# Kernel optimization log

Hardware: AMD Instinct MI355X
Metric: run time of the kernel (lower is better)

Reference implementation:

```python
import jax, jax.numpy as jnp
import numpy as np

B, T, C = 4, 2048, 768
H, D = 12, 64          # num_heads, head_size
R = 64                 # kv_lora_rank
ROPE_THETA = 10000.0


def setup_inputs() -> dict:
    key = jax.random.key(0)
    ks = jax.random.split(key, 8)
    s = lambda fan_in: 1.0 / np.sqrt(fan_in)
    return {
        "x":      jax.random.normal(ks[0], (B, T, C), jnp.float32),
        "Wq":     jax.random.normal(ks[1], (C, H * D), jnp.float32) * s(C),
        "Wdown":  jax.random.normal(ks[2], (C, R), jnp.float32) * s(C),
        "ln_g":   jnp.ones((R,), jnp.float32),
        "ln_b":   jnp.zeros((R,), jnp.float32),
        "Wup":    jax.random.normal(ks[3], (R, 2 * H * D), jnp.float32) * s(R),
        "Wo":     jax.random.normal(ks[4], (H * D, C), jnp.float32) * s(H * D),
        "bo":     jnp.zeros((C,), jnp.float32),
    }


def _rope_cos_sin(t, d, dtype):
    # freqs over half-dim, repeated twice (rotate-half convention)
    inv_freq = 1.0 / (ROPE_THETA ** (jnp.arange(0, d, 2, dtype=jnp.float32) / d))
    ang = jnp.arange(t, dtype=jnp.float32)[:, None] * inv_freq[None, :]  # [T, D/2]
    ang = jnp.concatenate([ang, ang], axis=-1)                            # [T, D]
    return jnp.cos(ang).astype(dtype), jnp.sin(ang).astype(dtype)


def _apply_rope(q, cos, sin):
    # q: [B, H, T, D]; cos/sin: [T, D]
    d2 = q.shape[-1] // 2
    rot = jnp.concatenate([-q[..., d2:], q[..., :d2]], axis=-1)
    return q * cos + rot * sin


def reference(x, Wq, Wdown, ln_g, ln_b, Wup, Wo, bo):
    b, t, c = x.shape
    q = (x @ Wq).reshape(b, t, H, D).transpose(0, 2, 1, 3)  # [B,H,T,D]

    ckv = x @ Wdown                                         # [B,T,R]
    mu = jnp.mean(ckv, axis=-1, keepdims=True)
    var = jnp.var(ckv, axis=-1, keepdims=True)
    ckv = (ckv - mu) * jax.lax.rsqrt(var + 1e-5) * ln_g + ln_b

    kv = (ckv @ Wup).reshape(b, t, 2, H, D)
    k = kv[:, :, 0].transpose(0, 2, 1, 3)                   # [B,H,T,D]
    v = kv[:, :, 1].transpose(0, 2, 1, 3)

    cos, sin = _rope_cos_sin(t, D, x.dtype)
    q = _apply_rope(q, cos, sin)
    k = _apply_rope(k, cos, sin)

    wei = jnp.einsum("bhqd,bhkd->bhqk", q, k) * (D ** -0.5)
    causal = jnp.tril(jnp.ones((t, t), bool))
    wei = jnp.where(causal, wei, -jnp.inf)
    wei = jax.nn.softmax(wei, axis=-1)                      # dropout: eval mode (identity)

    out = jnp.einsum("bhqk,bhkd->bhqd", wei, v)             # [B,H,T,D]
    out = out.transpose(0, 2, 1, 3).reshape(b, t, H * D)
    return out @ Wo + bo
```

## Files before the change

kernel.cpp:

```cpp
#include <hip/hip_runtime.h>
#include <hip/hip_bf16.h>
#include <math.h>

#define B_ 4
#define T_ 2048
#define C_ 768
#define H_ 12
#define D_ 64
#define R_ 64
#define BT_ (B_*T_)
#define HD_ (H_*D_)

typedef __attribute__((ext_vector_type(8))) short bf16x8;
typedef __attribute__((ext_vector_type(4))) float f32x4;
typedef __attribute__((ext_vector_type(16))) float f32x16;

__device__ inline short f2bf(float f) {
  union { float f; unsigned u; } x; x.f = f;
  unsigned r = x.u + 0x7fffu + ((x.u >> 16) & 1u);
  return (short)(r >> 16);
}
__device__ inline unsigned pk_bf16(float a, float b) {
#if __has_builtin(__builtin_amdgcn_cvt_pk_bf16_f32)
  auto t = __builtin_amdgcn_cvt_pk_bf16_f32(a, b);
  unsigned u; __builtin_memcpy(&u, &t, sizeof(unsigned)); return u;
#else
  union { float f; unsigned u; } x, y; x.f = a; y.f = b;
  unsigned ra = (x.u + 0x7fffu + ((x.u >> 16) & 1u)) >> 16;
  unsigned rb = (y.u + 0x7fffu + ((y.u >> 16) & 1u)) & 0xffff0000u;
  return ra | rb;
#endif
}
__device__ inline float fexp2(float x) {
#if __has_builtin(__builtin_amdgcn_exp2f)
  return __builtin_amdgcn_exp2f(x);
#else
  return exp2f(x);
#endif
}
typedef __attribute__((address_space(3))) unsigned lds_u32;
typedef __attribute__((address_space(1))) const unsigned glb_u32;
__device__ inline void gload_lds16(const void* g, void* l) {
  __builtin_amdgcn_global_load_lds((glb_u32*)g, (lds_u32*)l, 16, 0, 0);
}

__device__ inline void ttile(const float* __restrict__ src, short* __restrict__ dst,
                             int K, int N, int k0, int n0, int tid, float (*tl)[33]) {
  int tx = tid & 31, ty = tid >> 5;
  #pragma unroll
  for (int r = 0; r < 4; ++r)
    tl[ty + 8 * r][tx] = src[(size_t)(k0 + ty + 8 * r) * N + n0 + tx];
  __syncthreads();
  #pragma unroll
  for (int r = 0; r < 4; ++r)
    dst[(size_t)(n0 + ty + 8 * r) * K + k0 + tx] = f2bf(tl[tx][ty + 8 * r]);
}

#define NCONV (BT_*C_/4/256)

__global__ __launch_bounds__(256) void prep_conv(
    const float* __restrict__ x, short* __restrict__ x_bf,
    const float* __restrict__ Wq, const float* __restrict__ Wd,
    const float* __restrict__ Wup, const float* __restrict__ Wo,
    short* __restrict__ W1T, short* __restrict__ WupT, short* __restrict__ WoT,
    float* __restrict__ cs, float* __restrict__ sn) {
  __shared__ float tl[32][33];
  int tid = threadIdx.x;
  if (blockIdx.x < NCONV) {
    int i = blockIdx.x * 256 + tid;
    float4 v = ((const float4*)x)[i];
    short4 o;
    o.x = f2bf(v.x); o.y = f2bf(v.y); o.z = f2bf(v.z); o.w = f2bf(v.w);
    ((short4*)x_bf)[i] = o;
    return;
  }
  int blk = blockIdx.x - NCONV;
  if (blk < 576) {
    int tk = blk % 24, tn = blk / 24;
    ttile(Wq, W1T, 768, 768, tk * 32, tn * 32, tid, tl);
  } else if (blk < 624) {
    int l = blk - 576; int tk = l % 24, tn = l / 24;
    ttile(Wd, W1T + (size_t)768 * 768, 768, 64, tk * 32, tn * 32, tid, tl);
  } else if (blk < 720) {
    int l = blk - 624; int tk = l % 2, tn = l / 2;
    ttile(Wup, WupT, 64, 1536, tk * 32, tn * 32, tid, tl);
  } else if (blk < 1296) {
    int l = blk - 720; int tk = l % 24, tn = l / 24;
    ttile(Wo, WoT, 768, 768, tk * 32, tn * 32, tid, tl);
  } else {
    int base = (blk - 1296) * 1024;
    #pragma unroll
    for (int i = 0; i < 4; ++i) {
      int idx = base + tid + i * 256;
      int j = idx & 31, t = idx >> 5;
      float invf = exp2f(-(float)j * (13.287712379549449f / 32.f));
      float a = (float)t * invf;
      cs[idx] = cosf(a);
      sn[idx] = sinf(a);
    }
  }
}

#define SC2_ 0.18033688f

template<int MODE>
__global__ __launch_bounds__(256) void gemm64(
    const short* __restrict__ A, const short* __restrict__ Bt,
    int M, int N, int K,
    float* __restrict__ out0, const float* __restrict__ bias,
    const float* __restrict__ bias2,
    short* __restrict__ ob0, short* __restrict__ ob1,
    const float* __restrict__ cs, const float* __restrict__ sn)
{
  __shared__ short SM[128 * 64 + 64 * 64];
  short* As = SM;
  short* Bs = SM + 128 * 64;
  const int m0 = blockIdx.x * 128;
  const int n0 = blockIdx.y * 64;
  const int tid = threadIdx.x, lane = tid & 63, w = tid >> 6;
  const int fr = lane & 15, fk = (lane >> 4) * 8;
  const int rstage = lane >> 3;
  const int cstage = (lane & 7) * 8;

  f32x4 acc[2][4] = {};

  for (int k0 = 0; k0 < K; k0 += 64) {
    __syncthreads();
    #pragma unroll
    for (int i = 0; i < 4; ++i) {
      int c = w * 4 + i;
      int r = c * 8 + rstage;
      gload_lds16(&A[(size_t)(m0 + r) * K + k0 + cstage], &As[c * 512]);
    }
    #pragma unroll
    for (int i = 0; i < 2; ++i) {
      int c = w * 2 + i;
      int r = c * 8 + rstage;
      gload_lds16(&Bt[(size_t)(n0 + r) * K + k0 + cstage], &Bs[c * 512]);
    }
    __syncthreads();
    #pragma unroll
    for (int kk = 0; kk < 64; kk += 32) {
      bf16x8 a[2], b[4];
      a[0] = *(const bf16x8*)&As[(w * 32 +      fr) * 64 + kk + fk];
      a[1] = *(const bf16x8*)&As[(w * 32 + 16 + fr) * 64 + kk + fk];
      #pragma unroll
      for (int ni = 0; ni < 4; ++ni)
        b[ni] = *(const bf16x8*)&Bs[(ni * 16 + fr) * 64 + kk + fk];
      #pragma unroll
      for (int mi = 0; mi < 2; ++mi)
        #pragma unroll
        for (int ni = 0; ni < 4; ++ni)
          acc[mi][ni] = __builtin_amdgcn_mfma_f32_16x16x32_bf16(a[mi], b[ni], acc[mi][ni], 0, 0, 0);
    }
  }

  const int er = (lane >> 4) * 4, ec = lane & 15;

  if constexpr (MODE == 2) {
    #pragma unroll
    for (int mi = 0; mi < 2; ++mi)
      #pragma unroll
      for (int r = 0; r < 4; ++r) {
        int row = m0 + w * 32 + mi * 16 + er + r;
        #pragma unroll
        for (int ni = 0; ni < 4; ++ni) {
          int col = n0 + ni * 16 + ec;
          out0[(size_t)row * N + col] = acc[mi][ni][r] + bias[col];
        }
      }
    return;
  }

  if (n0 < 768) {
    int h = n0 >> 6;
    #pragma unroll
    for (int mi = 0; mi < 2; ++mi)
      #pragma unroll
      for (int r = 0; r < 4; ++r) {
        int row = m0 + w * 32 + mi * 16 + er + r;
        int t = row & (T_ - 1), bb = row >> 11;
        short* dst = ob0 + (((size_t)(bb * H_ + h)) * T_ + t) * 64;
        #pragma unroll
        for (int ni = 0; ni < 2; ++ni) {
          int d = ni * 16 + ec;
          float c = cs[t * 32 + d], s = sn[t * 32 + d];
          if constexpr (MODE == 0) { c *= SC2_; s *= SC2_; }
          float x0 = acc[mi][ni][r], x1 = acc[mi][ni + 2][r];
          dst[d]      = f2bf(x0 * c - x1 * s);
          dst[d + 32] = f2bf(x1 * c + x0 * s);
        }
      }
  } else if constexpr (MODE == 0) {
    #pragma unroll
    for (int mi = 0; mi < 2; ++mi)
      #pragma unroll
      for (int r = 0; r < 4; ++r) {
        float s = 0.f, s2 = 0.f;
        #pragma unroll
        for (int ni = 0; ni < 4; ++ni) { float v = acc[mi][ni][r]; s += v; s2 += v*v; }
        #pragma unroll
        for (int off = 1; off < 16; off <<= 1) {
          s  += __shfl_xor(s, off);
          s2 += __shfl_xor(s2, off);
        }
        float mu = s * (1.f/64.f);
        float var = s2 * (1.f/64.f) - mu * mu;
        float rstd = rsqrtf(var + 1e-5f);
        int row = m0 + w * 32 + mi * 16 + er + r;
        #pragma unroll
        for (int ni = 0; ni < 4; ++ni) {
          int d = ni * 16 + ec;
          ob1[(size_t)row * 64 + d] = f2bf((acc[mi][ni][r] - mu) * rstd * bias[d] + bias2[d]);
        }
      }
  } else {
    __syncthreads();
    short* Wl = SM + w * 2560;
    int h = (n0 - 768) >> 6;
    #pragma unroll
    for (int mi = 0; mi < 2; ++mi) {
      int tl0 = mi * 16 + er;
      #pragma unroll
      for (int ni = 0; ni < 4; ++ni) {
        int d = ni * 16 + ec;
        uint2 uu;
        uu.x = pk_bf16(acc[mi][ni][0], acc[mi][ni][1]);
        uu.y = pk_bf16(acc[mi][ni][2], acc[mi][ni][3]);
        *(uint2*)&Wl[d * 40 + tl0] = uu;
      }
    }
    int bb = m0 >> 11;
    int tg0 = (m0 & (T_ - 1)) + w * 32;
    int dl = lane >> 2, tl = (lane & 3) * 8;
    #pragma unroll
    for (int j = 0; j < 4; ++j) {
      int d = j * 16 + dl;
      uint4 vv = *(const uint4*)&Wl[d * 40 + tl];
      *(uint4*)&ob1[((size_t)(bb * H_ + h) * 64 + d) * T_ + tg0 + tl] = vv;
    }
  }
}

__global__ __launch_bounds__(256) void attn_mfma(
    const short* __restrict__ qgl, const short* __restrict__ kg,
    const short* __restrict__ vtg, short* __restrict__ o)
{
  __shared__ short Ks[8 * 512];
  __shared__ short Vts[8 * 512];
  __shared__ short Ps[4][32 * 72];

  const int bh = blockIdx.x;
  const int y  = blockIdx.y;
  const int qt1 = 31 - y, qt2 = y;
  const int tid = threadIdx.x, lane = tid & 63, w = tid >> 6;
  const int q32 = lane & 31, half = lane >> 5;
  short* Pw = Ps[w];
  const short* kb  = kg  + (size_t)bh * T_ * 64;
  const short* vtb = vtg + (size_t)bh * 64 * T_;
  const int b = bh / H_, h = bh - b * H_;

  const int qt_w = (w < 2) ? qt1 : qt2;
  const int q0 = qt_w * 64 + (w & 1) * 32;
  const int last_w = qt_w * 64;
  const int qidx = q0 + q32;

  const short* qrow = qgl + ((size_t)bh * T_ + qidx) * 64;
  bf16x8 bq[4];
  #pragma unroll
  for (int ks = 0; ks < 4; ++ks)
    bq[ks] = *(const bf16x8*)&qrow[ks * 16 + half * 8];

  f32x16 oacc[2] = {};
  float lrun = 0.f;
  const int kend = qt1 * 64;

  for (int kt = 0; kt <= kend; kt += 64) {
    __syncthreads();
    #pragma unroll
    for (int i = 0; i < 2; ++i) {
      int c = w * 2 + i;
      int kh = c >> 2, ks = c & 3;
      gload_lds16(kb + (size_t)(kt + kh * 32 + q32) * 64 + ks * 16 + half * 8, &Ks[c * 512]);
      gload_lds16(vtb + (size_t)(kh * 32 + q32) * T_ + kt + ks * 16 + half * 8, &Vts[c * 512]);
    }
    __syncthreads();

    if (kt > last_w) continue;
    const bool diag = (kt == last_w);
    const int dkh = diag ? (w & 1) : 2;
    const bool skip1 = diag && ((w & 1) == 0);

    float ls = 0.f;
    #pragma unroll
    for (int kh = 0; kh < 2; ++kh) {
      if (kh == 1 && skip1) break;
      f32x16 sacc = {};
      #pragma unroll
      for (int ks = 0; ks < 4; ++ks) {
        bf16x8 a = *(const bf16x8*)&Ks[(kh * 4 + ks) * 512 + lane * 8];
        sacc = __builtin_amdgcn_mfma_f32_32x32x16_bf16(a, bq[ks], sacc, 0, 0, 0);
      }
      float pv[16];
      if (kh != dkh) {
        #pragma unroll
        for (int r = 0; r < 16; ++r) { float p = fexp2(sacc[r]); pv[r] = p; ls += p; }
      } else {
        #pragma unroll
        for (int r = 0; r < 16; ++r) {
          int key = kt + kh * 32 + (r & 3) + 8 * (r >> 2) + 4 * half;
          float p = (key <= qidx) ? fexp2(sacc[r]) : 0.f;
          pv[r] = p; ls += p;
        }
      }
      #pragma unroll
      for (int g2 = 0; g2 < 4; ++g2) {
        uint2 uu;
        uu.x = pk_bf16(pv[4 * g2 + 0], pv[4 * g2 + 1]);
        uu.y = pk_bf16(pv[4 * g2 + 2], pv[4 * g2 + 3]);
        *(uint2*)&Pw[q32 * 72 + kh * 32 + 8 * g2 + 4 * half] = uu;
      }
    }
    ls += __shfl_xor(ls, 32);
    lrun += ls;

    const int ksmax = skip1 ? 2 : 4;
    for (int ks = 0; ks < ksmax; ++ks) {
      bf16x8 bp = *(const bf16x8*)&Pw[q32 * 72 + ks * 16 + half * 8];
      #pragma unroll
      for (int dt = 0; dt < 2; ++dt) {
        bf16x8 av = *(const bf16x8*)&Vts[(dt * 4 + ks) * 512 + lane * 8];
        oacc[dt] = __builtin_amdgcn_mfma_f32_32x32x16_bf16(av, bp, oacc[dt], 0, 0, 0);
      }
    }
  }

  float inv = 1.f / lrun;
  #pragma unroll
  for (int dt = 0; dt < 2; ++dt)
    #pragma unroll
    for (int g2 = 0; g2 < 4; ++g2) {
      uint2 uu;
      uu.x = pk_bf16(oacc[dt][4 * g2 + 0] * inv, oacc[dt][4 * g2 + 1] * inv);
      uu.y = pk_bf16(oacc[dt][4 * g2 + 2] * inv, oacc[dt][4 * g2 + 3] * inv);
      *(uint2*)&Pw[q32 * 72 + dt * 32 + 8 * g2 + 4 * half] = uu;
    }
  int row = lane >> 1, seg = lane & 1;
  int t = q0 + row;
  short* orow = o + ((size_t)(b * T_ + t)) * HD_ + h * 64 + seg * 32;
  #pragma unroll
  for (int i = 0; i < 4; ++i) {
    uint4 vv = *(const uint4*)&Pw[row * 72 + seg * 32 + i * 8];
    *(uint4*)&orow[i * 8] = vv;
  }
}

extern "C" void kernel_launch(void* const* d_in, const int* in_sizes, int n_in,
                              void* d_out, int out_size, void* d_ws, size_t ws_size,
                              hipStream_t stream) {
  (void)in_sizes; (void)n_in; (void)out_size; (void)ws_size;
  const float* x     = (const float*)d_in[0];
  const float* Wq    = (const float*)d_in[1];
  const float* Wdown = (const float*)d_in[2];
  const float* ln_g  = (const float*)d_in[3];
  const float* ln_b  = (const float*)d_in[4];
  const float* Wup   = (const float*)d_in[5];
  const float* Wo    = (const float*)d_in[6];
  const float* bo    = (const float*)d_in[7];
  float* out = (float*)d_out;

  char* w = (char*)d_ws;
  short* x_bf   = (short*)w;  w += (size_t)BT_ * C_    * 2;
  short* W1T    = (short*)w;  w += (size_t)832 * C_    * 2;
  short* WupT   = (short*)w;  w += (size_t)2*HD_ * R_  * 2;
  short* WoT    = (short*)w;  w += (size_t)HD_ * C_    * 2;
  short* ckv    = (short*)w;  w += (size_t)BT_ * R_    * 2;
  short* qb     = (short*)w;  w += (size_t)BT_ * HD_   * 2;
  short* kb     = (short*)w;  w += (size_t)BT_ * HD_   * 2;
  short* vt     = (short*)w;  w += (size_t)BT_ * HD_   * 2;
  short* att    = (short*)w;  w += (size_t)BT_ * HD_   * 2;
  float* cs_t   = (float*)w;  w += (size_t)T_ * 32 * 4;
  float* sn_t   = (float*)w;  w += (size_t)T_ * 32 * 4;

  prep_conv<<<NCONV + 1360, 256, 0, stream>>>(x, x_bf, Wq, Wdown, Wup, Wo,
                                              W1T, WupT, WoT, cs_t, sn_t);

  gemm64<0><<<dim3(BT_/128, 13), 256, 0, stream>>>(
      x_bf, W1T, BT_, 832, C_, nullptr, ln_g, ln_b, qb, ckv, cs_t, sn_t);

  gemm64<1><<<dim3(BT_/128, 24), 256, 0, stream>>>(
      ckv, WupT, BT_, 2*HD_, R_, nullptr, nullptr, nullptr, kb, vt, cs_t, sn_t);

  attn_mfma<<<dim3(B_*H_, 16), 256, 0, stream>>>(qb, kb, vt, att);

  gemm64<2><<<dim3(BT_/128, 12), 256, 0, stream>>>(
      att, WoT, BT_, C_, HD_, out, bo, nullptr, nullptr, nullptr, nullptr, nullptr);
}
```

Before: 207.0 us.

## Double-buffer K/V tiles and keep P in registers via permlane32 swap

Replaces the single K/V LDS buffers with a two-stage ring, so the global-to-LDS load for the next key tile is issued before computing the current one, and one barrier per iteration is dropped. The softmax probabilities are no longer round-tripped through LDS: they are packed to bf16 and rearranged across half-waves with permlane32_swap (with a shuffle fallback) into MFMA B-operand layout. It also adds s_setprio around the MFMA blocks and defers the cross-half row-sum reduction to the end. LDS footprint stays about the same, and the final output staging reuses the K/V buffer region.

After: 197.6 us. -4.5%, faster.

```diff
diff --git a/kernel.cpp b/kernel.cpp
--- a/kernel.cpp
+++ b/kernel.cpp
@@ -36,6 +36,19 @@
   return __builtin_amdgcn_exp2f(x);
 #else
   return exp2f(x);
+#endif
+}
+__device__ inline void pswap(unsigned &a, unsigned &b) {
+#if __has_builtin(__builtin_amdgcn_permlane32_swap)
+  auto r = __builtin_amdgcn_permlane32_swap((int)a, (int)b, false, false);
+  unsigned u[2]; __builtin_memcpy(u, &r, 8);
+  a = u[0]; b = u[1];
+#else
+  unsigned ax = __shfl_xor(a, 32), bx = __shfl_xor(b, 32);
+  bool hi = (threadIdx.x & 32) != 0;
+  unsigned na = hi ? bx : a;
+  unsigned nb = hi ? b : ax;
+  a = na; b = nb;
 #endif
 }
 typedef __attribute__((address_space(3))) unsigned lds_u32;
@@ -246,16 +259,13 @@
     const short* __restrict__ qgl, const short* __restrict__ kg,
     const short* __restrict__ vtg, short* __restrict__ o)
 {
-  __shared__ short Ks[8 * 512];
-  __shared__ short Vts[8 * 512];
-  __shared__ short Ps[4][32 * 72];
+  __shared__ short SMa[2][2][8 * 512];
 
   const int bh = blockIdx.x;
   const int y  = blockIdx.y;
   const int qt1 = 31 - y, qt2 = y;
   const int tid = threadIdx.x, lane = tid & 63, w = tid >> 6;
   const int q32 = lane & 31, half = lane >> 5;
-  short* Pw = Ps[w];
   const short* kb  = kg  + (size_t)bh * T_ * 64;
   const short* vtb = vtg + (size_t)bh * 64 * T_;
   const int b = bh / H_, h = bh - b * H_;
@@ -275,67 +285,96 @@
   float lrun = 0.f;
   const int kend = qt1 * 64;
 
-  for (int kt = 0; kt <= kend; kt += 64) {
-    __syncthreads();
+  auto stage = [&](int buf, int kt) {
     #pragma unroll
     for (int i = 0; i < 2; ++i) {
       int c = w * 2 + i;
       int kh = c >> 2, ks = c & 3;
-      gload_lds16(kb + (size_t)(kt + kh * 32 + q32) * 64 + ks * 16 + half * 8, &Ks[c * 512]);
-      gload_lds16(vtb + (size_t)(kh * 32 + q32) * T_ + kt + ks * 16 + half * 8, &Vts[c * 512]);
-    }
+      gload_lds16(kb + (size_t)(kt + kh * 32 + q32) * 64 + ks * 16 + half * 8,
+                  &SMa[buf][0][c * 512]);
+      gload_lds16(vtb + (size_t)(kh * 32 + q32) * T_ + kt + ks * 16 + half * 8,
+                  &SMa[buf][1][c * 512]);
+    }
+  };
+
+  stage(0, 0);
+  __syncthreads();
+
+  int cur = 0;
+  for (int kt = 0; kt <= kend; kt += 64) {
+    if (kt + 64 <= kend) stage(cur ^ 1, kt + 64);
+
+    if (kt <= last_w) {
+      const short* Kc = &SMa[cur][0][0];
+      const short* Vc = &SMa[cur][1][0];
+      const bool diag = (kt == last_w);
+      const int dkh = diag ? (w & 1) : 2;
+      const bool skip1 = diag && ((w & 1) == 0);
+
+      bf16x8 bp[4];
+      #pragma unroll
+      for (int kh = 0; kh < 2; ++kh) {
+        if (kh == 1 && skip1) break;
+        f32x16 sacc = {};
+        __builtin_amdgcn_s_setprio(1);
+        #pragma unroll
+        for (int ks = 0; ks < 4; ++ks) {
+          bf16x8 a = *(const bf16x8*)&Kc[(kh * 4 + ks) * 512 + lane * 8];
+          sacc = __builtin_amdgcn_mfma_f32_32x32x16_bf16(a, bq[ks], sacc, 0, 0, 0);
+        }
+        __builtin_amdgcn_s_setprio(0);
+        float pv[16];
+        if (kh != dkh) {
+          #pragma unroll
+          for (int r = 0; r < 16; ++r) { float p = fexp2(sacc[r]); pv[r] = p; lrun += p; }
+        } else {
+          #pragma unroll
+          for (int r = 0; r < 16; ++r) {
+            int key = kt + kh * 32 + (r & 3) + 8 * (r >> 2) + 4 * half;
+            float p = (key <= qidx) ? fexp2(sacc[r]) : 0.f;
+            pv[r] = p; lrun += p;
+          }
+        }
+        unsigned l0 = pk_bf16(pv[0],  pv[1]),  h0 = pk_bf16(pv[2],  pv[3]);
+        unsigned l1 = pk_bf16(pv[4],  pv[5]),  h1 = pk_bf16(pv[6],  pv[7]);
+        unsigned l2 = pk_bf16(pv[8],  pv[9]),  h2 = pk_bf16(pv[10], pv[11]);
+        unsigned l3 = pk_bf16(pv[12], pv[13]), h3 = pk_bf16(pv[14], pv[15]);
+        pswap(l0, l1); pswap(h0, h1);
+        pswap(l2, l3); pswap(h2, h3);
+        union { unsigned u[4]; bf16x8 v; } f0, f1;
+        f0.u[0] = l0; f0.u[1] = h0; f0.u[2] = l1; f0.u[3] = h1;
+        f1.u[0] = l2; f1.u[1] = h2; f1.u[2] = l3; f1.u[3] = h3;
+        bp[2 * kh + 0] = f0.v;
+        bp[2 * kh + 1] = f1.v;
+      }
+
+      __builtin_amdgcn_s_setprio(1);
+      #pragma unroll
+      for (int ks = 0; ks < 2; ++ks)
+        #pragma unroll
+        for (int dt = 0; dt < 2; ++dt) {
+          bf16x8 av = *(const bf16x8*)&Vc[(dt * 4 + ks) * 512 + lane * 8];
+          oacc[dt] = __builtin_amdgcn_mfma_f32_32x32x16_bf16(av, bp[ks], oacc[dt], 0, 0, 0);
+        }
+      if (!skip1) {
+        #pragma unroll
+        for (int ks = 2; ks < 4; ++ks)
+          #pragma unroll
+          for (int dt = 0; dt < 2; ++dt) {
+            bf16x8 av = *(const bf16x8*)&Vc[(dt * 4 + ks) * 512 + lane * 8];
+            oacc[dt] = __builtin_amdgcn_mfma_f32_32x32x16_bf16(av, bp[ks], oacc[dt], 0, 0, 0);
+          }
+      }
+      __builtin_amdgcn_s_setprio(0);
+    }
+
     __syncthreads();
-
-    if (kt > last_w) continue;
-    const bool diag = (kt == last_w);
-    const int dkh = diag ? (w & 1) : 2;
-    const bool skip1 = diag && ((w & 1) == 0);
-
-    float ls = 0.f;
-    #pragma unroll
-    for (int kh = 0; kh < 2; ++kh) {
-      if (kh == 1 && skip1) break;
-      f32x16 sacc = {};
-      #pragma unroll
-      for (int ks = 0; ks < 4; ++ks) {
-        bf16x8 a = *(const bf16x8*)&Ks[(kh * 4 + ks) * 512 + lane * 8];
-        sacc = __builtin_amdgcn_mfma_f32_32x32x16_bf16(a, bq[ks], sacc, 0, 0, 0);
-      }
-      float pv[16];
-      if (kh != dkh) {
-        #pragma unroll
-        for (int r = 0; r < 16; ++r) { float p = fexp2(sacc[r]); pv[r] = p; ls += p; }
-      } else {
-        #pragma unroll
-        for (int r = 0; r < 16; ++r) {
-          int key = kt + kh * 32 + (r & 3) + 8 * (r >> 2) + 4 * half;
-          float p = (key <= qidx) ? fexp2(sacc[r]) : 0.f;
-          pv[r] = p; ls += p;
-        }
-      }
-      #pragma unroll
-      for (int g2 = 0; g2 < 4; ++g2) {
-        uint2 uu;
-        uu.x = pk_bf16(pv[4 * g2 + 0], pv[4 * g2 + 1]);
-        uu.y = pk_bf16(pv[4 * g2 + 2], pv[4 * g2 + 3]);
-        *(uint2*)&Pw[q32 * 72 + kh * 32 + 8 * g2 + 4 * half] = uu;
-      }
-    }
-    ls += __shfl_xor(ls, 32);
-    lrun += ls;
-
-    const int ksmax = skip1 ? 2 : 4;
-    for (int ks = 0; ks < ksmax; ++ks) {
-      bf16x8 bp = *(const bf16x8*)&Pw[q32 * 72 + ks * 16 + half * 8];
-      #pragma unroll
-      for (int dt = 0; dt < 2; ++dt) {
-        bf16x8 av = *(const bf16x8*)&Vts[(dt * 4 + ks) * 512 + lane * 8];
-        oacc[dt] = __builtin_amdgcn_mfma_f32_32x32x16_bf16(av, bp, oacc[dt], 0, 0, 0);
-      }
-    }
-  }
-
-  float inv = 1.f / lrun;
+    cur ^= 1;
+  }
+
+  float ltot = lrun + __shfl_xor(lrun, 32);
+  float inv = 1.f / ltot;
+  short* Pw = &SMa[0][0][0] + w * 2304;
   #pragma unroll
   for (int dt = 0; dt < 2; ++dt)
     #pragma unroll
```
